# Performance work log

Measured on AMD Instinct MI355X. Metric: run time of the kernel, lower is better.

## Reference

```python
import jax, jax.numpy as jnp
import numpy as np
from jax import lax

V = 9; C1 = 80; C2 = 40; C4 = 24; CH = 32
H1, W1 = 30, 40; H2, W2 = 60, 80; H4, W4 = 120, 160
SHAPE = (96, 96, 96); N = 131072; EPS = 1e-5
OFFS = np.stack(np.meshgrid(np.arange(-1, 2), np.arange(-1, 2), np.arange(-1, 2), indexing='ij'), -1).reshape(-1, 3).astype(np.int32)  # 27 kernel offsets


def conv2d(x, w, b):
    y = lax.conv_general_dilated(x, w, (1, 1), 'SAME', dimension_numbers=('NCHW', 'OIHW', 'NCHW'))
    return y + b[None, :, None, None]


def bn1d(x, g, b):  # eval-mode BatchNorm1d (running_mean=0, running_var=1)
    return g * x * (1.0 / np.sqrt(1.0 + EPS)) + b


def layernorm(x, g, b):
    m = x.mean(-1, keepdims=True)
    v = ((x - m) ** 2).mean(-1, keepdims=True)
    return (x - m) / jnp.sqrt(v + EPS) * g + b


def grid_sample_zeros(img, gx, gy):
    # img [V,C,H,W]; gx,gy [V,M] normalized to [-1,1]; bilinear, align_corners=True, zeros padding
    Vn, C, H, W = img.shape
    px = (gx + 1.0) * 0.5 * (W - 1)
    py = (gy + 1.0) * 0.5 * (H - 1)
    x0 = jnp.floor(px); y0 = jnp.floor(py)
    wx = px - x0; wy = py - y0
    flat = img.reshape(Vn, C, H * W)
    def corner(xc, yc, wgt):
        valid = (xc >= 0) & (xc <= W - 1) & (yc >= 0) & (yc <= H - 1)
        xi = jnp.clip(xc, 0, W - 1).astype(jnp.int32)
        yi = jnp.clip(yc, 0, H - 1).astype(jnp.int32)
        idx = yi * W + xi  # [V,M]
        g = jax.vmap(lambda f, i: f[:, i])(flat, idx)  # [V,C,M]
        return g * (wgt * valid)[:, None, :]
    return (corner(x0, y0, (1 - wx) * (1 - wy)) + corner(x0 + 1, y0, wx * (1 - wy))
            + corner(x0, y0 + 1, (1 - wx) * wy) + corner(x0 + 1, y0 + 1, wx * wy))


def subm_conv(feat, W3, cxyz, grid):
    # submanifold sparse 3x3x3 conv: per-offset gather of active neighbors -> GEMM -> accumulate
    n = feat.shape[0]
    shp = jnp.asarray(SHAPE, jnp.int32)
    out = jnp.zeros((n, W3.shape[-1]), feat.dtype)
    for k in range(27):
        nc = cxyz + jnp.asarray(OFFS[k])
        inb = jnp.all((nc >= 0) & (nc < shp), axis=1)
        ncc = jnp.clip(nc, 0, shp - 1)
        idx = grid[ncc[:, 0], ncc[:, 1], ncc[:, 2]]
        ok = (inb & (idx >= 0)).astype(feat.dtype)
        g = feat[jnp.clip(idx, 0, n - 1)] * ok[:, None]
        out = out + g @ W3[k]
    return out


def _forward(feats_1x, feats_2x, feats_4x, origin, voxel_size, KRcam,
             w_f1, b_f1, w_f2, b_f2, w_f4, b_f4, w_down, b_down,
             w_p1, b_p1, w_p2, b_p2, w_p3, b_p3, w_p4, b_p4,
             bn0_g, bn0_b, w_elan, w_s1, ln1_g, ln1_b, w_s2, ln2_g, ln2_b,
             w_s3, ln3_g, ln3_b, w_s4, bn4_g, bn4_b,
             coords, stage, min_view_number):
    # feat_fusion_pre (bs=1, take batch 0)
    f1 = jax.nn.relu(conv2d(feats_1x[:, 0], w_f1, b_f1))
    f2 = jax.nn.relu(conv2d(feats_2x[:, 0], w_f2, b_f2))
    f4 = jax.nn.relu(conv2d(feats_4x[:, 0], w_f4, b_f4))
    f1 = jax.image.resize(f1, (V, C1, H2, W2), 'bilinear')  # F.interpolate x2
    f4 = f4.reshape(V, C4, H2, 2, W2, 2).mean(axis=(3, 5))  # AvgPool2d(2)
    fuse = jnp.concatenate([f1, f2, f4], axis=1)
    fuse = jax.nn.relu(conv2d(fuse, w_down, b_down))
    for w, b in ((w_p1, b_p1), (w_p2, b_p2), (w_p3, b_p3), (w_p4, b_p4)):
        fuse = fuse + jax.nn.relu(conv2d(fuse, w, b))  # residual blocks -> [V,CH,H2,W2]
    # multi-view projection
    cxyz = coords[:, 1:]
    world = cxyz.astype(jnp.float32) * voxel_size + origin[0]
    hom = jnp.concatenate([world, jnp.ones_like(world[:, :1])], axis=1)  # [N,4]
    im_p = jnp.einsum('vij,nj->vin', KRcam[:, 0], hom)  # [V,3,N]
    im_z = im_p[:, 2]
    gx = 2.0 * (im_p[:, 0] / im_z) / (W4 - 1) - 1.0
    gy = 2.0 * (im_p[:, 1] / im_z) / (H4 - 1) - 1.0
    mask = (jnp.abs(gx) <= 1) & (jnp.abs(gy) <= 1) & (im_z > 0)  # [V,N]
    count = mask.sum(0).astype(jnp.float32)
    # inputs are constructed so every voxel is seen by all views: valid_voxel compaction == identity
    feats = grid_sample_zeros(fuse, gx, gy) * mask[:, None, :]  # [V,CH,N]
    feat = feats.transpose(2, 0, 1)  # [N,V,CH]
    m = mask.T.astype(feat.dtype)  # [N,V]
    den = m.sum(1, keepdims=True)
    mean = (m[..., None] * feat).sum(1) / den
    var = (m[..., None] * (feat - mean[:, None, :]) ** 2).sum(1) / den  # [N,CH]
    # sparse subm conv chain
    sc = cxyz // (2 ** (2 - stage))  # stage=2 -> identity
    grid = jnp.full(SHAPE, -1, jnp.int32).at[sc[:, 0], sc[:, 1], sc[:, 2]].set(jnp.arange(N, dtype=jnp.int32))
    x = bn1d(var, bn0_g, bn0_b)
    x = jax.nn.relu(subm_conv(x, w_elan, sc, grid))  # Spares3dELAN stand-in
    r = jax.nn.relu(subm_conv(x, w_s1, sc, grid)); x = layernorm(r + x, ln1_g, ln1_b)
    r = jax.nn.relu(subm_conv(x, w_s2, sc, grid)); x = layernorm(r + x, ln2_g, ln2_b)
    r = jax.nn.relu(subm_conv(x, w_s3, sc, grid)); x = layernorm(r + x, ln3_g, ln3_b)
    occ = bn1d(subm_conv(x, w_s4, sc, grid), bn4_g, bn4_b)  # [N,1]
    return occ, coords, count


def setup_inputs() -> dict:
    key = jax.random.key(0)
    keys = jax.random.split(key, 40)
    ki = iter(range(40))
    def rn(shape, s=1.0):
        return jax.random.normal(keys[next(ki)], shape, jnp.float32) * s
    inp = {}
    inp['feats_1x'] = rn((V, 1, C1, H1, W1))
    inp['feats_2x'] = rn((V, 1, C2, H2, W2))
    inp['feats_4x'] = rn((V, 1, C4, H4, W4))
    flat = np.arange(N, dtype=np.int64) * 6  # unique active voxels in a 96^3 grid
    cx = flat // (96 * 96); rem = flat % (96 * 96)
    inp['coords'] = jnp.asarray(np.stack([np.zeros(N, np.int64), cx, rem // 96, rem % 96], 1), jnp.int32)
    inp['origin'] = jnp.asarray([[-1.92, -1.92, 1.0]], jnp.float32)
    inp['voxel_size'] = jnp.float32(0.04)
    fx, fy = 38.0, 28.0
    P = np.zeros((V, 1, 3, 4), np.float32)
    for v in range(V):
        P[v, 0] = np.array([[fx, 0.0, (W4 - 1) / 2, fx * 0.02 * (v - 4)],
                            [0.0, fy, (H4 - 1) / 2, 0.0],
                            [0.0, 0.0, 1.0, 0.0]], np.float32)
    inp['KRcam'] = jnp.asarray(P)
    s = 0.05
    inp['w_f1'] = rn((C1, C1, 3, 3), s); inp['b_f1'] = rn((C1,), s)
    inp['w_f2'] = rn((C2, C2, 3, 3), s); inp['b_f2'] = rn((C2,), s)
    inp['w_f4'] = rn((C4, C4, 3, 3), s); inp['b_f4'] = rn((C4,), s)
    inp['w_down'] = rn((CH, C1 + C2 + C4, 1, 1), s); inp['b_down'] = rn((CH,), s)
    for i in (1, 2, 3, 4):
        inp['w_p%d' % i] = rn((CH, CH, 3, 3), s); inp['b_p%d' % i] = rn((CH,), s)
    inp['bn0_g'] = jnp.ones((CH,), jnp.float32); inp['bn0_b'] = jnp.zeros((CH,), jnp.float32)
    inp['w_elan'] = rn((27, CH, CH), s)
    inp['w_s1'] = rn((27, CH, CH), s); inp['ln1_g'] = jnp.ones((CH,), jnp.float32); inp['ln1_b'] = jnp.zeros((CH,), jnp.float32)
    inp['w_s2'] = rn((27, CH, CH), s); inp['ln2_g'] = jnp.ones((CH,), jnp.float32); inp['ln2_b'] = jnp.zeros((CH,), jnp.float32)
    inp['w_s3'] = rn((27, CH, CH), s); inp['ln3_g'] = jnp.ones((CH,), jnp.float32); inp['ln3_b'] = jnp.zeros((CH,), jnp.float32)
    inp['w_s4'] = rn((27, CH, 1), s); inp['bn4_g'] = jnp.ones((1,), jnp.float32); inp['bn4_b'] = jnp.zeros((1,), jnp.float32)
    inp['stage'] = 2
    inp['min_view_number'] = 1
    return inp


def reference(feats_1x, feats_2x, feats_4x, origin, voxel_size, KRcam,
              w_f1, b_f1, w_f2, b_f2, w_f4, b_f4, w_down, b_down,
              w_p1, b_p1, w_p2, b_p2, w_p3, b_p3, w_p4, b_p4,
              bn0_g, bn0_b, w_elan, w_s1, ln1_g, ln1_b, w_s2, ln2_g, ln2_b,
              w_s3, ln3_g, ln3_b, w_s4, bn4_g, bn4_b,
              coords, stage, min_view_number):
    return _forward(feats_1x, feats_2x, feats_4x, origin, voxel_size, KRcam,
                    w_f1, b_f1, w_f2, b_f2, w_f4, b_f4, w_down, b_down,
                    w_p1, b_p1, w_p2, b_p2, w_p3, b_p3, w_p4, b_p4,
                    bn0_g, bn0_b, w_elan, w_s1, ln1_g, ln1_b, w_s2, ln2_g, ln2_b,
                    w_s3, ln3_g, ln3_b, w_s4, bn4_g, bn4_b,
                    coords, stage, min_view_number)
```

## Files before the change

### kernel.cpp

```cpp
#include <hip/hip_runtime.h>
#include <math.h>

#define VN 9
#define NVOX 131072
#define GS 96
static constexpr float INVS = 0.9999950000374997f;

typedef short bf16x8 __attribute__((ext_vector_type(8)));
typedef float f32x4v __attribute__((ext_vector_type(4)));

__device__ inline float4 ld4(const float* p){ return *reinterpret_cast<const float4*>(p); }

__device__ inline ushort f2b(float f){
  unsigned u = __float_as_uint(f);
  unsigned r = (u + 0x7fffu + ((u >> 16) & 1u)) >> 16;
  return (ushort)r;
}
__device__ inline float b2f(ushort s){ return __uint_as_float(((unsigned)s) << 16); }
__device__ inline float blo(unsigned u){ return __uint_as_float(u << 16); }
__device__ inline float bhi(unsigned u){ return __uint_as_float(u & 0xffff0000u); }

__device__ inline float4 ld4b(const ushort* p){
  uint2 u = *reinterpret_cast<const uint2*>(p);
  float4 r; r.x = blo(u.x); r.y = bhi(u.x); r.z = blo(u.y); r.w = bhi(u.y); return r;
// ... 60 lines not shown
}

__global__ __launch_bounds__(256) void k_prep(
    const float* wf1s, const float* wf2s, const float* wf4s, const float* wdns,
    const float* wp0s, const float* wp1s, const float* wp2s, const float* wp3s,
    const float* wes, const float* ws1s, const float* ws2s, const float* ws3s,
    ushort* wf1, ushort* wf2, ushort* wf4, ushort* wdn,
    ushort* wp0, ushort* wp1, ushort* wp2, ushort* wp3,
    ushort* w2e, ushort* w2s1, ushort* w2s2, ushort* w2s3,
    int* grid,
    const float* f1, const float* f2, const float* f4,
    ushort* o1, ushort* o2, ushort* o4){
  __shared__ float lds[96*65];
  int bid = blockIdx.x;
  int tx = threadIdx.x;
  if (bid < 270){ int t = bid*256+tx; if (t < 69120) wprep2_dev(wf1s, wf1, 80, 80, 3, 3, 80, t); return; }
  bid -= 270;
  if (bid < 108){ int t = bid*256+tx; if (t < 27648) wprep2_dev(wf2s, wf2, 40, 40, 3, 2, 48, t); return; }
  bid -= 108;
  if (bid < 36){ int t = bid*256+tx; if (t < 9216) wprep2_dev(wf4s, wf4, 24, 24, 3, 1, 32, t); return; }
  bid -= 36;
  if (bid < 20){ int t = bid*256+tx; if (t < 5120) wprep2_dev(wdns, wdn, 32, 144, 1, 5, 32, t); return; }
  bid -= 20;
  if (bid < 36){ int t = bid*256+tx; if (t < 9216) wprep2_dev(wp0s, wp0, 32, 32, 3, 1, 32, t); return; }
  bid -= 36;
  if (bid < 36){ int t = bid*256+tx; if (t < 9216) wprep2_dev(wp1s, wp1, 32, 32, 3, 1, 32, t); return; }
  bid -= 36;
  if (bid < 36){ int t = bid*256+tx; if (t < 9216) wprep2_dev(wp2s, wp2, 32, 32, 3, 1, 32, t); return; }
  bid -= 36;
  if (bid < 36){ int t = bid*256+tx; if (t < 9216) wprep2_dev(wp3s, wp3, 32, 32, 3, 1, 32, t); return; }
  bid -= 36;
  if (bid < 108){ int t = bid*256+tx; if (t < 27648) wprep_dev(wes, w2e, t); return; }
  bid -= 108;
  if (bid < 108){ int t = bid*256+tx; if (t < 27648) wprep_dev(ws1s, w2s1, t); return; }
  bid -= 108;
  if (bid < 108){ int t = bid*256+tx; if (t < 27648) wprep_dev(ws2s, w2s2, t); return; }
  bid -= 108;
  if (bid < 108){ int t = bid*256+tx; if (t < 27648) wprep_dev(ws3s, w2s3, t); return; }
  bid -= 108;
  if (bid < 3456){ int t = bid*256+tx; if (t < GS*GS*GS) grid[t] = -1; return; }
  bid -= 3456;
  if (bid < 171){ nhwc_tile_dev(f1, o1, 80, 96, 1200, bid, 19, lds, tx); return; }
  bid -= 171;
  if (bid < 675){ nhwc_tile_dev(f2, o2, 40, 64, 4800, bid, 75, lds, tx); return; }
  bid -= 675;
  if (bid < 2700){ nhwc_tile_dev(f4, o4, 24, 32, 19200, bid, 300, lds, tx); }
}

template<int CK, int NT, int TAPS, int MT>
__device__ void conv_dev(
    const ushort* __restrict__ fin, const ushort* __restrict__ w2,
    const float* __restrict__ bias, ushort* __restrict__ outp,
    int H, int W, int total, int Cout, int outStride, int outOff,
    const ushort* __restrict__ skipin, int bid, int tid){
  constexpr int CIN = CK*32;
  constexpr int COP = NT*16;
  int lane = tid & 63;
  int wave = tid >> 6;
  int vbase = bid*(MT*64) + wave*(MT*16);
  int m = lane & 15, q = lane >> 4;
  int HW = H*W;
  int p[MT], py[MT], px[MT]; bool pin[MT];
  #pragma unroll
  for (int t = 0; t < MT; ++t){
    int pp = vbase + t*16 + m;
    pin[t] = pp < total;
    if (pp > total-1) pp = total-1;
    p[t] = pp;
    int v = pp / HW; int rem = pp - v*HW;
    int y = rem / W;
    py[t] = y; px[t] = rem - y*W;
  }
  f32x4v acc[MT][NT];
  #pragma unroll
  for (int t = 0; t < MT; ++t)
    #pragma unroll
    for (int n = 0; n < NT; ++n) acc[t][n] = 0.f;
  bf16x8 z = (short)0;

  #pragma unroll 1
  for (int tap = 0; tap < TAPS; ++tap){
    int dy = (TAPS == 9) ? tap/3 - 1 : 0;
    int dx = (TAPS == 9) ? tap%3 - 1 : 0;
    int off = dy*W + dx;
    bool val[MT];
    #pragma unroll
    for (int t = 0; t < MT; ++t)
      val[t] = pin[t] && ((unsigned)(py[t]+dy) < (unsigned)H)
                      && ((unsigned)(px[t]+dx) < (unsigned)W);
    #pragma unroll
    for (int ck = 0; ck < CK; ++ck){
      bf16x8 Af[MT], Bf[NT];
      #pragma unroll
      for (int t = 0; t < MT; ++t){
        size_t idx = val[t] ? (size_t)(p[t]+off) : 0;
        bf16x8 a = *(const bf16x8*)(fin + idx*CIN + ck*32 + q*8);
        Af[t] = val[t] ? a : z;
      }
      #pragma unroll
      for (int n = 0; n < NT; ++n)
        Bf[n] = *(const bf16x8*)(w2 + ((size_t)((tap*CK+ck)*COP + n*16 + m))*32 + q*8);
      #pragma unroll
      for (int t = 0; t < MT; ++t)
        #pragma unroll
        for (int n = 0; n < NT; ++n)
          acc[t][n] = __builtin_amdgcn_mfma_f32_16x16x32_bf16(Af[t], Bf[n], acc[t][n], 0, 0, 0);
    }
  }

  #pragma unroll
  for (int n = 0; n < NT; ++n){
    int co = n*16 + m;
    bool cok = co < Cout;
    float bs = cok ? bias[co] : 0.f;
    #pragma unroll
    for (int t = 0; t < MT; ++t){
      #pragma unroll
      for (int r = 0; r < 4; ++r){
        int pp = vbase + t*16 + q*4 + r;
        if (pp < total && cok){
          float x = fmaxf(acc[t][n][r] + bs, 0.f);
          if (skipin) x += b2f(skipin[(size_t)pp*CIN + co]);
          outp[(size_t)pp*outStride + outOff + co] = f2b(x);
        }
      }
    }
  }
}

template<int CK, int NT, int TAPS, int MT>
__global__ __launch_bounds__(256) void k_conv_mfma(
    const ushort* __restrict__ fin, const ushort* __restrict__ w2,
    const float* __restrict__ bias, ushort* __restrict__ outp,
    int H, int W, int total, int Cout, int outStride, int outOff,
    const ushort* __restrict__ skipin){
  conv_dev<CK,NT,TAPS,MT>(fin, w2, bias, outp, H, W, total, Cout, outStride, outOff,
                          skipin, blockIdx.x, threadIdx.x);
}

template<int TH, int NT>
__device__ void conv_lds_dev(
    const ushort* __restrict__ fin, const ushort* __restrict__ w2,
    const float* __restrict__ bias, ushort* __restrict__ outp,
    int H, int W, int Cout, int outStride,
    const ushort* __restrict__ skipin, ushort* lds, int bid, int tid){
  constexpr int RPW = TH/4;
  constexpr int PS = 36;
  int xtiles = W >> 4;
  int ytiles = (H + TH - 1) / TH;
  int v  = bid / (ytiles*xtiles);
  int rem = bid - v*(ytiles*xtiles);
  int ty = (rem / xtiles) * TH;
  int tx = (rem % xtiles) * 16;
  const ushort* ibase = fin + (size_t)v*H*W*32;
  for (int i = tid; i < (TH+2)*18*4; i += 256){
    int chunk = i & 3;
    int pxi = i >> 2;
    int ly = pxi / 18, lx = pxi - ly*18;
    int gy = ty + ly - 1, gx = tx + lx - 1;
    uint4 d = {0,0,0,0};
    if ((unsigned)gy < (unsigned)H && (unsigned)gx < (unsigned)W)
      d = *(const uint4*)(ibase + ((size_t)gy*W + gx)*32 + chunk*8);
    *(uint4*)(lds + (size_t)(ly*18 + lx)*PS + chunk*8) = d;
  }
  __syncthreads();
  int lane = tid & 63;
  int wave = tid >> 6;
  int m = lane & 15, q = lane >> 4;
  f32x4v acc[RPW][NT];
  #pragma unroll
  for (int t = 0; t < RPW; ++t)
    #pragma unroll
    for (int n = 0; n < NT; ++n) acc[t][n] = 0.f;

  #pragma unroll 1
  for (int tap = 0; tap < 9; ++tap){
    int dy = tap/3 - 1, dx = tap%3 - 1;
    bf16x8 Af[RPW], Bf[NT];
    #pragma unroll
    for (int t = 0; t < RPW; ++t){
      int ly = wave*RPW + t + 1 + dy;
      int lx = m + 1 + dx;
      Af[t] = *(const bf16x8*)(lds + (size_t)(ly*18 + lx)*PS + q*8);
    }
    #pragma unroll
    for (int n = 0; n < NT; ++n)
      Bf[n] = *(const bf16x8*)(w2 + ((size_t)(tap*(NT*16) + n*16 + m))*32 + q*8);
    #pragma unroll
    for (int t = 0; t < RPW; ++t)
      #pragma unroll
      for (int n = 0; n < NT; ++n)
        acc[t][n] = __builtin_amdgcn_mfma_f32_16x16x32_bf16(Af[t], Bf[n], acc[t][n], 0, 0, 0);
  }

  #pragma unroll
  for (int n = 0; n < NT; ++n){
    int co = n*16 + m;
    bool cok = co < Cout;
    float bs = cok ? bias[co] : 0.f;
    #pragma unroll
    for (int t = 0; t < RPW; ++t){
      int y = ty + wave*RPW + t;
      #pragma unroll
      for (int r = 0; r < 4; ++r){
        int x = tx + q*4 + r;
        if (y < H && cok){
          size_t pp = (size_t)(v*H + y)*W + x;
          float val = fmaxf(acc[t][n][r] + bs, 0.f);
          if (skipin) val += b2f(skipin[pp*32 + co]);
          outp[pp*outStride + co] = f2b(val);
        }
      }
    }
  }
}

__global__ __launch_bounds__(256) void k_conv_lds4(
    const ushort* __restrict__ fin, const ushort* __restrict__ w2,
    const float* __restrict__ bias, ushort* __restrict__ outp,
    const ushort* __restrict__ skipin){
  __shared__ ushort lds[6*18*36];
  conv_lds_dev<4,2>(fin, w2, bias, outp, 60, 80, 32, 32, skipin, lds, blockIdx.x, threadIdx.x);
}

__device__ void scatter_dev(const int* __restrict__ coords, const int* __restrict__ stage,
                            int* __restrict__ grid, int* __restrict__ scn,
                            float* __restrict__ coords_out,
                            const float* __restrict__ origin, const float* __restrict__ vsz,
                            const float* __restrict__ KR,
                            ushort* __restrict__ sidx, uint2* __restrict__ sw,
                            float* __restrict__ cnt, int n){
  int c0 = coords[n*4], c1 = coords[n*4+1], c2 = coords[n*4+2], c3 = coords[n*4+3];
  coords_out[n*4+0] = (float)c0;
  coords_out[n*4+1] = (float)c1;
  coords_out[n*4+2] = (float)c2;
  coords_out[n*4+3] = (float)c3;
  int sh = 2 - stage[0];
  int s1 = c1 >> sh, s2 = c2 >> sh, s3 = c3 >> sh;
  scn[n*3+0] = s1; scn[n*3+1] = s2; scn[n*3+2] = s3;
  grid[(s1*GS + s2)*GS + s3] = n;

  float vs = vsz[0];
  float wx = (float)c1*vs + origin[0];
  float wy = (float)c2*vs + origin[1];
  float wz = (float)c3*vs + origin[2];
  float den = 0.f;
  #pragma unroll 1
  for (int v = 0; v < VN; ++v){
    const float* P = KR + v*12;
    float ix = P[0]*wx + P[1]*wy + P[2]*wz + P[3];
    float iy = P[4]*wx + P[5]*wy + P[6]*wz + P[7];
    float iz = P[8]*wx + P[9]*wy + P[10]*wz + P[11];
    float gx = 2.f*(ix/iz)/159.f - 1.f;
    float gy = 2.f*(iy/iz)/119.f - 1.f;
    bool ok = (fabsf(gx) <= 1.f) && (fabsf(gy) <= 1.f) && (iz > 0.f);
    float px = ok ? (gx + 1.f)*0.5f*79.f : 0.f;
    float py = ok ? (gy + 1.f)*0.5f*59.f : 0.f;
    float x0f = floorf(px), y0f = floorf(py);
    float fx = px - x0f, fy = py - y0f;
    int idx = (int)y0f*80 + (int)x0f;
    float mf = ok ? 1.f : 0.f;
    float w00 = (1.f-fx)*(1.f-fy)*mf, w01 = fx*(1.f-fy)*mf;
    float w10 = (1.f-fx)*fy*mf,       w11 = fx*fy*mf;
    uint2 s;
    s.x = (unsigned)f2b(w00) | ((unsigned)f2b(w01) << 16);
    s.y = (unsigned)f2b(w10) | ((unsigned)f2b(w11) << 16);
    sidx[(size_t)v*NVOX + n] = (ushort)idx;
    sw[(size_t)v*NVOX + n] = s;
    den += mf;
  }
  cnt[n] = den;
}

__global__ __launch_bounds__(256) void k_heads(
    const ushort* nhwc1, const ushort* wf1, const float* b_f1, ushort* t1,
    const ushort* nhwc2, const ushort* wf2, const float* b_f2, ushort* fcat,
    const ushort* nhwc4, const ushort* wf4, const float* b_f4, ushort* t4,
    const int* coords, const int* stage, int* grid, int* scn, float* coords_out,
    const float* origin, const float* vsz, const float* KR,
    ushort* sidx, uint2* sw, float* cnt){
  __shared__ ushort lds[18*18*36];
  int bid = blockIdx.x;
  int tid = threadIdx.x;
  if (bid < 169){ conv_dev<3,5,9,1>(nhwc1, wf1, b_f1, t1, 30, 40, 10800, 80, 80, 0, nullptr, bid, tid); return; }
  bid -= 169;
  if (bid < 720){ conv_lds_dev<16,2>(nhwc4, wf4, b_f4, t4, 120, 160, 24, 24, nullptr, lds, bid, tid); return; }
  bid -= 720;
  if (bid < 675){ conv_dev<2,3,9,1>(nhwc2, wf2, b_f2, fcat, 60, 80, 43200, 40, 160, 80, nullptr, bid, tid); return; }
  bid -= 675;
  { int n = bid*256 + tid;
    scatter_dev(coords, stage, grid, scn, coords_out, origin, vsz, KR, sidx, sw, cnt, n); }
}

__global__ __launch_bounds__(256) void k_respool_nbr(
    const ushort* __restrict__ t1, const ushort* __restrict__ t4, ushort* __restrict__ fc,
    const int* __restrict__ scn, const int* __restrict__ grid,
    int* __restrict__ nbr, unsigned* __restrict__ gmask16){
  __shared__ unsigned m16[4];
  int bid = blockIdx.x;
  int tidx = threadIdx.x;
  if (bid < 5063){
    int tid = bid*256 + tidx;
    if (tid < 864000){
      int c4 = tid % 20;
      int x  = (tid / 20) % 80;
      int y  = (tid / 1600) % 60;
      int v  = tid / 96000;
      int c = c4*4;
      int ky = y >> 1; int y0, y1; float wy0, wy1;
      if ((y & 1) == 0){ y0 = ky-1; y1 = ky; wy0 = 0.25f; wy1 = 0.75f; if (y0 < 0){ y0 = 0; wy0 = 0.f; wy1 = 1.f; } }
      else             { y0 = ky; y1 = ky+1; wy0 = 0.75f; wy1 = 0.25f; if (y1 > 29){ y1 = 29; wy1 = 0.f; wy0 = 1.f; } }
      int kx = x >> 1; int x0, x1; float wx0, wx1;
      if ((x & 1) == 0){ x0 = kx-1; x1 = kx; wx0 = 0.25f; wx1 = 0.75f; if (x0 < 0){ x0 = 0; wx0 = 0.f; wx1 = 1.f; } }
      else             { x0 = kx; x1 = kx+1; wx0 = 0.75f; wx1 = 0.25f; if (x1 > 39){ x1 = 39; wx1 = 0.f; wx0 = 1.f; } }
      float4 a00 = ld4b(t1 + ((size_t)(v*30 + y0)*40 + x0)*80 + c);
      float4 a01 = ld4b(t1 + ((size_t)(v*30 + y0)*40 + x1)*80 + c);
      float4 a10 = ld4b(t1 + ((size_t)(v*30 + y1)*40 + x0)*80 + c);
      float4 a11 = ld4b(t1 + ((size_t)(v*30 + y1)*40 + x1)*80 + c);
      float w00 = wy0*wx0, w01 = wy0*wx1, w10 = wy1*wx0, w11 = wy1*wx1;
      float4 r;
      r.x = w00*a00.x + w01*a01.x + w10*a10.x + w11*a11.x;
      r.y = w00*a00.y + w01*a01.y + w10*a10.y + w11*a11.y;
      r.z = w00*a00.z + w01*a01.z + w10*a10.z + w11*a11.z;
      r.w = w00*a00.w + w01*a01.w + w10*a10.w + w11*a11.w;
      st4b(fc + ((size_t)(v*60 + y)*80 + x)*160 + c, r);
      return;
    }
    int t = tid - 864000;
    if (t >= 432000) return;
    int c4 = t % 10;
    int x  = (t / 10) % 80;
    int y  = (t / 800) % 60;
    int v  = t / 48000;
    if (c4 < 6){
      int c = c4*4;
      const ushort* b0 = t4 + ((size_t)(v*120 + 2*y)*160 + 2*x)*24 + c;
      float4 a = ld4b(b0), b = ld4b(b0 + 24), cc = ld4b(b0 + 160*24), d = ld4b(b0 + 160*24 + 24);
      float4 r;
      r.x = 0.25f*(a.x + b.x + cc.x + d.x);
      r.y = 0.25f*(a.y + b.y + cc.y + d.y);
      r.z = 0.25f*(a.z + b.z + cc.z + d.z);
      r.w = 0.25f*(a.w + b.w + cc.w + d.w);
      st4b(fc + ((size_t)(v*60 + y)*80 + x)*160 + 120 + c, r);
    } else {
      float4 zz = {0.f,0.f,0.f,0.f};
      st4b(fc + ((size_t)(v*60 + y)*80 + x)*160 + 144 + (c4-6)*4, zz);
    }
    return;
  }
  bid -= 5063;
  if (tidx < 4) m16[tidx] = 0;
  __syncthreads();
  int vb = bid*64;
  int lane = tidx & 63;
  int wv = tidx >> 6;
  int n = vb + lane;
  int sx = scn[n*3+0], sy = scn[n*3+1], sz = scn[n*3+2];
  int k0 = wv*7;
  int k1 = min(27, k0 + 7);
  unsigned msk = 0;
  #pragma unroll 1
  for (int k = k0; k < k1; ++k){
    int dx = k/9 - 1, dy = (k/3)%3 - 1, dz = k%3 - 1;
    int nx = sx+dx, ny = sy+dy, nz = sz+dz;
    int idx = -1;
    if (((unsigned)nx < 96u) && ((unsigned)ny < 96u) && ((unsigned)nz < 96u))
      idx = grid[(nx*GS + ny)*GS + nz];
    unsigned long long b = __ballot(idx >= 0);
    unsigned sub = (unsigned)((b >> ((lane >> 4)*16)) & 0xFFFFull);
    if (sub){
      nbr[(size_t)k*NVOX + n] = idx;
      msk |= (1u << k);
    }
  }
  if ((lane & 15) == 0 && msk) atomicOr(&m16[lane >> 4], msk);
  __syncthreads();
  if (tidx < 4) gmask16[(vb >> 4) + tidx] = m16[tidx];
}

__global__ __launch_bounds__(256) void k_sample(
    const ushort* __restrict__ fuse, const ushort* __restrict__ sidx,
    const uint2* __restrict__ sw,
    const float* __restrict__ cnt, const float* __restrict__ bn0g,
    const float* __restrict__ bn0b, ushort* __restrict__ F0){
  int tid = blockIdx.x*256 + threadIdx.x;
  int vox = tid >> 3;
  int c4 = tid & 7;
  int c = c4*4;
  int si[VN]; uint2 wv[VN];
  #pragma unroll
  for (int v = 0; v < VN; ++v){
    si[v] = sidx[(size_t)v*NVOX + vox];
    wv[v] = sw[(size_t)v*NVOX + vox];
  }
  float s0=0.f,s1=0.f,s2=0.f,s3=0.f;
  float q0=0.f,q1=0.f,q2=0.f,q3=0.f;
  #pragma unroll
  for (int v = 0; v < VN; ++v){
    float w00 = blo(wv[v].x), w01 = bhi(wv[v].x);
    float w10 = blo(wv[v].y), w11 = bhi(wv[v].y);
    const ushort* bp = fuse + (size_t)v*153600 + (size_t)si[v]*32 + c;
    float4 a00 = ld4b(bp);
    float4 a01 = ld4b(bp + 32);
    float4 a10 = ld4b(bp + 2560);
    float4 a11 = ld4b(bp + 2592);
    float g0 = w00*a00.x + w01*a01.x + w10*a10.x + w11*a11.x;
    float g1 = w00*a00.y + w01*a01.y + w10*a10.y + w11*a11.y;
    float g2 = w00*a00.z + w01*a01.z + w10*a10.z + w11*a11.z;
    float g3 = w00*a00.w + w01*a01.w + w10*a10.w + w11*a11.w;
    s0 += g0; q0 += g0*g0;
    s1 += g1; q1 += g1*g1;
    s2 += g2; q2 += g2*g2;
    s3 += g3; q3 += g3*g3;
  }
  float iden = 1.f/cnt[vox];
  float m0 = s0*iden, m1 = s1*iden, m2 = s2*iden, m3 = s3*iden;
  float4 g = ld4(bn0g + c);
  float4 b = ld4(bn0b + c);
  float4 r;
  r.x = g.x*fmaxf(q0*iden - m0*m0, 0.f)*INVS + b.x;
  r.y = g.y*fmaxf(q1*iden - m1*m1, 0.f)*INVS + b.y;
  r.z = g.z*fmaxf(q2*iden - m2*m2, 0.f)*INVS + b.z;
  r.w = g.w*fmaxf(q3*iden - m3*m3, 0.f)*INVS + b.w;
  st4b(F0 + (size_t)vox*32 + c, r);
}

template<int MODE>
__global__ __launch_bounds__(256, 4) void k_subm_mfma(
    const ushort* __restrict__ fin, const ushort* __restrict__ w2,
    const int* __restrict__ nbr, const unsigned* __restrict__ gmask16,
    const float* __restrict__ lng, const float* __restrict__ lnb,
    ushort* __restrict__ fout){
  int lane = threadIdx.x & 63;
  int wave = threadIdx.x >> 6;
  int vb = blockIdx.x*128 + wave*32;
  int m = lane & 15;
  int q = lane >> 4;

  unsigned rem0 = gmask16[(vb >> 4) + 0];
  unsigned rem1 = gmask16[(vb >> 4) + 1];
  unsigned rem = rem0 | rem1;

  f32x4v acc[2][2];
  acc[0][0] = 0.f; acc[0][1] = 0.f; acc[1][0] = 0.f; acc[1][1] = 0.f;
  bf16x8 zc = (short)0;

  while (rem){
    int k0 = __ffs(rem) - 1; rem &= rem - 1;
    int k1 = -1, k2 = -1;
    if (rem){ k1 = __ffs(rem) - 1; rem &= rem - 1; }
    if (rem){ k2 = __ffs(rem) - 1; rem &= rem - 1; }
    int a0v = nbr[(size_t)k0*NVOX + vb + m];
    int b0v = nbr[(size_t)k0*NVOX + vb + 16 + m];
    int a1 = -1, b1 = -1, a2 = -1, b2 = -1;
    if (k1 >= 0){
      int av = nbr[(size_t)k1*NVOX + vb + m];
      int bv = nbr[(size_t)k1*NVOX + vb + 16 + m];
      a1 = ((rem0 >> k1) & 1) ? av : -1;
      b1 = ((rem1 >> k1) & 1) ? bv : -1;
    }
    if (k2 >= 0){
      int av = nbr[(size_t)k2*NVOX + vb + m];
      int bv = nbr[(size_t)k2*NVOX + vb + 16 + m];
      a2 = ((rem0 >> k2) & 1) ? av : -1;
      b2 = ((rem1 >> k2) & 1) ? bv : -1;
    }
    int a0 = ((rem0 >> k0) & 1) ? a0v : -1;
    int b0 = ((rem1 >> k0) & 1) ? b0v : -1;
    bf16x8 A0, B0, A1 = zc, B1 = zc, A2 = zc, B2 = zc, t;
    bf16x8 w10 = zc, w11 = zc, w20 = zc, w21 = zc;
    t = *(const bf16x8*)(fin + (size_t)(a0 < 0 ? 0 : a0)*32 + q*8); A0 = (a0 < 0) ? zc : t;
    t = *(const bf16x8*)(fin + (size_t)(b0 < 0 ? 0 : b0)*32 + q*8); B0 = (b0 < 0) ? zc : t;
    bf16x8 w00 = *(const bf16x8*)(w2 + (size_t)(k0*32 + m)*32 + q*8);
    bf16x8 w01 = *(const bf16x8*)(w2 + (size_t)(k0*32 + 16 + m)*32 + q*8);
    if (k1 >= 0){
      t = *(const bf16x8*)(fin + (size_t)(a1 < 0 ? 0 : a1)*32 + q*8); A1 = (a1 < 0) ? zc : t;
      t = *(const bf16x8*)(fin + (size_t)(b1 < 0 ? 0 : b1)*32 + q*8); B1 = (b1 < 0) ? zc : t;
      w10 = *(const bf16x8*)(w2 + (size_t)(k1*32 + m)*32 + q*8);
      w11 = *(const bf16x8*)(w2 + (size_t)(k1*32 + 16 + m)*32 + q*8);
    }
    if (k2 >= 0){
      t = *(const bf16x8*)(fin + (size_t)(a2 < 0 ? 0 : a2)*32 + q*8); A2 = (a2 < 0) ? zc : t;
      t = *(const bf16x8*)(fin + (size_t)(b2 < 0 ? 0 : b2)*32 + q*8); B2 = (b2 < 0) ? zc : t;
      w20 = *(const bf16x8*)(w2 + (size_t)(k2*32 + m)*32 + q*8);
      w21 = *(const bf16x8*)(w2 + (size_t)(k2*32 + 16 + m)*32 + q*8);
    }
    acc[0][0] = __builtin_amdgcn_mfma_f32_16x16x32_bf16(A0, w00, acc[0][0], 0, 0, 0);
    acc[0][1] = __builtin_amdgcn_mfma_f32_16x16x32_bf16(A0, w01, acc[0][1], 0, 0, 0);
    acc[1][0] = __builtin_amdgcn_mfma_f32_16x16x32_bf16(B0, w00, acc[1][0], 0, 0, 0);
    acc[1][1] = __builtin_amdgcn_mfma_f32_16x16x32_bf16(B0, w01, acc[1][1], 0, 0, 0);
    if (k1 >= 0){
      acc[0][0] = __builtin_amdgcn_mfma_f32_16x16x32_bf16(A1, w10, acc[0][0], 0, 0, 0);
      acc[0][1] = __builtin_amdgcn_mfma_f32_16x16x32_bf16(A1, w11, acc[0][1], 0, 0, 0);
      acc[1][0] = __builtin_amdgcn_mfma_f32_16x16x32_bf16(B1, w10, acc[1][0], 0, 0, 0);
      acc[1][1] = __builtin_amdgcn_mfma_f32_16x16x32_bf16(B1, w11, acc[1][1], 0, 0, 0);
    }
    if (k2 >= 0){
      acc[0][0] = __builtin_amdgcn_mfma_f32_16x16x32_bf16(A2, w20, acc[0][0], 0, 0, 0);
      acc[0][1] = __builtin_amdgcn_mfma_f32_16x16x32_bf16(A2, w21, acc[0][1], 0, 0, 0);
      acc[1][0] = __builtin_amdgcn_mfma_f32_16x16x32_bf16(B2, w20, acc[1][0], 0, 0, 0);
      acc[1][1] = __builtin_amdgcn_mfma_f32_16x16x32_bf16(B2, w21, acc[1][1], 0, 0, 0);
    }
  }

  int ch0 = m, ch1 = 16 + m;
  float g0 = 0.f, g1 = 0.f, bb0 = 0.f, bb1 = 0.f;
  if (MODE == 1){ g0 = lng[ch0]; g1 = lng[ch1]; bb0 = lnb[ch0]; bb1 = lnb[ch1]; }
  #pragma unroll
  for (int t = 0; t < 2; ++t){
    #pragma unroll
    for (int r = 0; r < 4; ++r){
      int vox = vb + t*16 + q*4 + r;
      float x0 = fmaxf(acc[t][0][r], 0.f);
      float x1 = fmaxf(acc[t][1][r], 0.f);
      if (MODE == 1){
        x0 += b2f(fin[(size_t)vox*32 + ch0]);
        x1 += b2f(fin[(size_t)vox*32 + ch1]);
        float s = x0 + x1;
        s += __shfl_xor(s, 1, 16);
        s += __shfl_xor(s, 2, 16);
        s += __shfl_xor(s, 4, 16);
        s += __shfl_xor(s, 8, 16);
        float mean = s * (1.f/32.f);
        float d0 = x0 - mean, d1 = x1 - mean;
        float v2 = d0*d0 + d1*d1;
        v2 += __shfl_xor(v2, 1, 16);
        v2 += __shfl_xor(v2, 2, 16);
        v2 += __shfl_xor(v2, 4, 16);
        v2 += __shfl_xor(v2, 8, 16);
        float rs = 1.f / sqrtf(v2*(1.f/32.f) + 1e-5f);
        x0 = d0*rs*g0 + bb0;
        x1 = d1*rs*g1 + bb1;
      }
      fout[(size_t)vox*32 + ch0] = f2b(x0);
      fout[(size_t)vox*32 + ch1] = f2b(x1);
    }
  }
}

__global__ __launch_bounds__(256) void k_s4(
    const ushort* __restrict__ fin, const float* __restrict__ w4,
    const int* __restrict__ nbr, const unsigned* __restrict__ gmask16,
    const float* __restrict__ bn4g, const float* __restrict__ bn4b,
    float* __restrict__ occ){
  int tid = blockIdx.x*256 + threadIdx.x;
  int n = tid >> 2;
  int part = tid & 3;
  unsigned rem = gmask16[n >> 4];
  float acc = 0.f;
  while (rem){
    int k0 = __ffs(rem) - 1; rem &= rem - 1;
    int k1 = -1;
    if (rem){ k1 = __ffs(rem) - 1; rem &= rem - 1; }
    int i0 = nbr[(size_t)k0*NVOX + n];
    int i1 = (k1 >= 0) ? nbr[(size_t)k1*NVOX + n] : -1;
    uint4 d0 = *(const uint4*)(fin + (size_t)(i0 < 0 ? 0 : i0)*32 + part*8);
    uint4 d1 = {0,0,0,0};
    if (k1 >= 0) d1 = *(const uint4*)(fin + (size_t)(i1 < 0 ? 0 : i1)*32 + part*8);
    if (i0 >= 0){
      float4 wa = ld4(w4 + k0*32 + part*8);
      float4 wb = ld4(w4 + k0*32 + part*8 + 4);
      acc += blo(d0.x)*wa.x + bhi(d0.x)*wa.y + blo(d0.y)*wa.z + bhi(d0.y)*wa.w
           + blo(d0.z)*wb.x + bhi(d0.z)*wb.y + blo(d0.w)*wb.z + bhi(d0.w)*wb.w;
    }
    if (i1 >= 0){
      float4 wa = ld4(w4 + k1*32 + part*8);
      float4 wb = ld4(w4 + k1*32 + part*8 + 4);
      acc += blo(d1.x)*wa.x + bhi(d1.x)*wa.y + blo(d1.y)*wa.z + bhi(d1.y)*wa.w
           + blo(d1.z)*wb.x + bhi(d1.z)*wb.y + blo(d1.w)*wb.z + bhi(d1.w)*wb.w;
    }
  }
  acc += __shfl_xor(acc, 1, 4);
  acc += __shfl_xor(acc, 2, 4);
  if (part == 0) occ[n] = bn4g[0]*acc*INVS + bn4b[0];
}

extern "C" void kernel_launch(void* const* d_in, const int* in_sizes, int n_in,
                              void* d_out, int out_size, void* d_ws, size_t ws_size,
                              hipStream_t stream){
  const float* feats1 = (const float*)d_in[0];
  const float* feats2 = (const float*)d_in[1];
  const float* feats4 = (const float*)d_in[2];
  const int*   coords = (const int*)d_in[3];
  const float* origin = (const float*)d_in[4];
  const float* vsz    = (const float*)d_in[5];
  const float* KR     = (const float*)d_in[6];
  const float* w_f1 = (const float*)d_in[7];  const float* b_f1 = (const float*)d_in[8];
  const float* w_f2 = (const float*)d_in[9];  const float* b_f2 = (const float*)d_in[10];
  const float* w_f4 = (const float*)d_in[11]; const float* b_f4 = (const float*)d_in[12];
  const float* w_dn = (const float*)d_in[13]; const float* b_dn = (const float*)d_in[14];
  const float* w_p[4] = {(const float*)d_in[15], (const float*)d_in[17],
                         (const float*)d_in[19], (const float*)d_in[21]};
  const float* b_p[4] = {(const float*)d_in[16], (const float*)d_in[18],
                         (const float*)d_in[20], (const float*)d_in[22]};
  const float* bn0g = (const float*)d_in[23]; const float* bn0b = (const float*)d_in[24];
  const float* w_elan = (const float*)d_in[25];
  const float* w_s1 = (const float*)d_in[26]; const float* ln1g = (const float*)d_in[27]; const float* ln1b = (const float*)d_in[28];
  const float* w_s2 = (const float*)d_in[29]; const float* ln2g = (const float*)d_in[30]; const float* ln2b = (const float*)d_in[31];
  const float* w_s3 = (const float*)d_in[32]; const float* ln3g = (const float*)d_in[33]; const float* ln3b = (const float*)d_in[34];
  const float* w_s4 = (const float*)d_in[35]; const float* bn4g = (const float*)d_in[36]; const float* bn4b = (const float*)d_in[37];
  const int* stage  = (const int*)d_in[38];
  float* out = (float*)d_out;
  char* base = (char*)d_ws;

  size_t off = 0;
  auto alloc = [&](size_t bytes)->char*{ char* p = base + off; off += (bytes + 255) & ~(size_t)255; return p; };
  ushort* nhwc1 = (ushort*)alloc((size_t)9*30*40*96*2);
  ushort* nhwc2 = (ushort*)alloc((size_t)9*60*80*64*2);
  ushort* nhwc4 = (ushort*)alloc((size_t)9*120*160*32*2);
  ushort* t1    = (ushort*)alloc((size_t)9*30*40*80*2);
  ushort* t4    = (ushort*)alloc((size_t)9*120*160*24*2);
  ushort* fcat  = (ushort*)alloc((size_t)9*60*80*160*2);
  ushort* A     = (ushort*)alloc((size_t)9*60*80*32*2);
  ushort* B     = (ushort*)alloc((size_t)9*60*80*32*2);
  ushort* Fb0   = (ushort*)alloc((size_t)NVOX*32*2);
  ushort* Fb1   = (ushort*)alloc((size_t)NVOX*32*2);
  int*    nbr   = (int*)alloc((size_t)27*NVOX*4);
  int*    grid  = (int*)alloc((size_t)GS*GS*GS*4);
  int*    scn   = (int*)alloc((size_t)NVOX*3*4);
  unsigned* gmask16 = (unsigned*)alloc((size_t)(NVOX/16)*4);
  ushort* wf1   = (ushort*)alloc(9*3*80*32*2);
  ushort* wf2   = (ushort*)alloc(9*2*48*32*2);
  ushort* wf4   = (ushort*)alloc(9*1*32*32*2);
  ushort* wdn   = (ushort*)alloc(1*5*32*32*2);
  ushort* wp0   = (ushort*)alloc(9*1*32*32*2);
  ushort* wp1   = (ushort*)alloc(9*1*32*32*2);
  ushort* wp2   = (ushort*)alloc(9*1*32*32*2);
  ushort* wp3   = (ushort*)alloc(9*1*32*32*2);
  ushort* w2e   = (ushort*)alloc(27*1024*2);
  ushort* w2s1  = (ushort*)alloc(27*1024*2);
  ushort* w2s2  = (ushort*)alloc(27*1024*2);
  ushort* w2s3  = (ushort*)alloc(27*1024*2);
  ushort* sidx  = (ushort*)alloc((size_t)VN*NVOX*2);
  uint2*  sw    = (uint2*)alloc((size_t)VN*NVOX*8);

  auto nb = [](int total){ return (total + 255)/256; };

  k_prep<<<8012,256,0,stream>>>(
      w_f1, w_f2, w_f4, w_dn, w_p[0], w_p[1], w_p[2], w_p[3],
      w_elan, w_s1, w_s2, w_s3,
      wf1, wf2, wf4, wdn, wp0, wp1, wp2, wp3, w2e, w2s1, w2s2, w2s3, grid,
      feats1, feats2, feats4, nhwc1, nhwc2, nhwc4);

  k_heads<<<169 + 720 + 675 + 512,256,0,stream>>>(
      nhwc1, wf1, b_f1, t1,
      nhwc2, wf2, b_f2, fcat,
      nhwc4, wf4, b_f4, t4,
      coords, stage, grid, scn, out + NVOX,
      origin, vsz, KR, sidx, sw, out + 5*NVOX);

  k_respool_nbr<<<5063 + 2048,256,0,stream>>>(t1, t4, fcat, scn, grid, nbr, gmask16);

  k_conv_mfma<5,2,1,1><<<675,256,0,stream>>>(fcat, wdn, b_dn, A, 60, 80, 43200, 32, 32, 0, nullptr);
  k_conv_lds4<<<675,256,0,stream>>>(A, wp0, b_p[0], B, A);
  k_conv_lds4<<<675,256,0,stream>>>(B, wp1, b_p[1], A, B);
  k_conv_lds4<<<675,256,0,stream>>>(A, wp2, b_p[2], B, A);
  k_conv_lds4<<<675,256,0,stream>>>(B, wp3, b_p[3], A, B);

  k_sample<<<NVOX/32,256,0,stream>>>(A, sidx, sw, out + 5*NVOX, bn0g, bn0b, Fb0);

  k_subm_mfma<0><<<NVOX/128,256,0,stream>>>(Fb0, w2e,  nbr, gmask16, nullptr, nullptr, Fb1);
  k_subm_mfma<1><<<NVOX/128,256,0,stream>>>(Fb1, w2s1, nbr, gmask16, ln1g, ln1b, Fb0);
  k_subm_mfma<1><<<NVOX/128,256,0,stream>>>(Fb0, w2s2, nbr, gmask16, ln2g, ln2b, Fb1);
  k_subm_mfma<1><<<NVOX/128,256,0,stream>>>(Fb1, w2s3, nbr, gmask16, ln3g, ln3b, Fb0);

  k_s4<<<NVOX/64,256,0,stream>>>(Fb0, w_s4, nbr, gmask16, bn4g, bn4b, out);
}
```

Measured before the change: 343.9 us.

## Transpose MFMA operands for vectorized epilogues; recompute sample weights inline

The MFMA operand order is swapped in the dense conv, LDS conv and sparse subm kernels. Each lane now holds four consecutive output channels for one pixel or voxel, so the epilogues do 8-byte bf16 vector stores, vector bias/LN-parameter loads and vector skip loads instead of scalar strided ones. The LayerNorm reduction now uses two cross-quad shuffles instead of four. Separately, the scatter stage no longer precomputes and stores the bilinear sample indices and weights; k_sample recomputes the projection per voxel. This removes a global write/read round trip of sidx/sw at the cost of redundant projection math across the 8 threads sharing a voxel.

New measurement: 345.2 us. No clear change (+0.4%).

```diff
diff --git a/kernel.cpp b/kernel.cpp
--- a/kernel.cpp
+++ b/kernel.cpp
@@ -136,7 +136,7 @@
     const ushort* __restrict__ fin, const ushort* __restrict__ w2,
     const float* __restrict__ bias, ushort* __restrict__ outp,
     int H, int W, int total, int Cout, int outStride, int outOff,
-    const ushort* __restrict__ skipin, int bid, int tid){
+    int bid, int tid){
   constexpr int CIN = CK*32;
   constexpr int COP = NT*16;
   int lane = tid & 63;
@@ -188,25 +188,25 @@
       for (int t = 0; t < MT; ++t)
         #pragma unroll
         for (int n = 0; n < NT; ++n)
-          acc[t][n] = __builtin_amdgcn_mfma_f32_16x16x32_bf16(Af[t], Bf[n], acc[t][n], 0, 0, 0);
+          acc[t][n] = __builtin_amdgcn_mfma_f32_16x16x32_bf16(Bf[n], Af[t], acc[t][n], 0, 0, 0);
     }
   }
 
   #pragma unroll
   for (int n = 0; n < NT; ++n){
-    int co = n*16 + m;
-    bool cok = co < Cout;
-    float bs = cok ? bias[co] : 0.f;
+    int co4 = n*16 + q*4;
+    bool cok = co4 < Cout;
+    float4 bs = cok ? ld4(bias + co4) : float4{0.f,0.f,0.f,0.f};
     #pragma unroll
     for (int t = 0; t < MT; ++t){
-      #pragma unroll
-      for (int r = 0; r < 4; ++r){
-        int pp = vbase + t*16 + q*4 + r;
-        if (pp < total && cok){
-          float x = fmaxf(acc[t][n][r] + bs, 0.f);
-          if (skipin) x += b2f(skipin[(size_t)pp*CIN + co]);
-          outp[(size_t)pp*outStride + outOff + co] = f2b(x);
-        }
+      int pp = vbase + t*16 + m;
+      if (pp < total && cok){
+        float4 v;
+        v.x = fmaxf(acc[t][n][0] + bs.x, 0.f);
+        v.y = fmaxf(acc[t][n][1] + bs.y, 0.f);
+        v.z = fmaxf(acc[t][n][2] + bs.z, 0.f);
+        v.w = fmaxf(acc[t][n][3] + bs.w, 0.f);
+        st4b(outp + (size_t)pp*outStride + outOff + co4, v);
       }
     }
   }
@@ -216,10 +216,9 @@
 __global__ __launch_bounds__(256) void k_conv_mfma(
     const ushort* __restrict__ fin, const ushort* __restrict__ w2,
     const float* __restrict__ bias, ushort* __restrict__ outp,
-    int H, int W, int total, int Cout, int outStride, int outOff,
-    const ushort* __restrict__ skipin){
+    int H, int W, int total, int Cout, int outStride, int outOff){
   conv_dev<CK,NT,TAPS,MT>(fin, w2, bias, outp, H, W, total, Cout, outStride, outOff,
-                          skipin, blockIdx.x, threadIdx.x);
+                          blockIdx.x, threadIdx.x);
 }
 
 template<int TH, int NT>
@@ -274,26 +273,30 @@
     for (int t = 0; t < RPW; ++t)
       #pragma unroll
       for (int n = 0; n < NT; ++n)
-        acc[t][n] = __builtin_amdgcn_mfma_f32_16x16x32_bf16(Af[t], Bf[n], acc[t][n], 0, 0, 0);
+        acc[t][n] = __builtin_amdgcn_mfma_f32_16x16x32_bf16(Bf[n], Af[t], acc[t][n], 0, 0, 0);
   }
 
   #pragma unroll
   for (int n = 0; n < NT; ++n){
-    int co = n*16 + m;
-    bool cok = co < Cout;
-    float bs = cok ? bias[co] : 0.f;
+    int co4 = n*16 + q*4;
+    bool cok = co4 < Cout;
+    float4 bs = cok ? ld4(bias + co4) : float4{0.f,0.f,0.f,0.f};
     #pragma unroll
     for (int t = 0; t < RPW; ++t){
       int y = ty + wave*RPW + t;
-      #pragma unroll
-      for (int r = 0; r < 4; ++r){
-        int x = tx + q*4 + r;
-        if (y < H && cok){
-          size_t pp = (size_t)(v*H + y)*W + x;
-          float val = fmaxf(acc[t][n][r] + bs, 0.f);
-          if (skipin) val += b2f(skipin[pp*32 + co]);
-          outp[pp*outStride + co] = f2b(val);
+      int x = tx + m;
+      if (y < H && cok){
+        size_t pp = (size_t)(v*H + y)*W + x;
+        float4 val;
+        val.x = fmaxf(acc[t][n][0] + bs.x, 0.f);
+        val.y = fmaxf(acc[t][n][1] + bs.y, 0.f);
+        val.z = fmaxf(acc[t][n][2] + bs.z, 0.f);
+        val.w = fmaxf(acc[t][n][3] + bs.w, 0.f);
+        if (skipin){
+          float4 sk = ld4b(skipin + pp*32 + co4);
+          val.x += sk.x; val.y += sk.y; val.z += sk.z; val.w += sk.w;
         }
+        st4b(outp + pp*outStride + co4, val);
       }
     }
   }
@@ -312,7 +315,6 @@
                             float* __restrict__ coords_out,
                             const float* __restrict__ origin, const float* __restrict__ vsz,
                             const float* __restrict__ KR,
-                            ushort* __restrict__ sidx, uint2* __restrict__ sw,
                             float* __restrict__ cnt, int n){
   int c0 = coords[n*4], c1 = coords[n*4+1], c2 = coords[n*4+2], c3 = coords[n*4+3];
   coords_out[n*4+0] = (float)c0;
@@ -338,20 +340,7 @@
     float gx = 2.f*(ix/iz)/159.f - 1.f;
     float gy = 2.f*(iy/iz)/119.f - 1.f;
     bool ok = (fabsf(gx) <= 1.f) && (fabsf(gy) <= 1.f) && (iz > 0.f);
-    float px = ok ? (gx + 1.f)*0.5f*79.f : 0.f;
-    float py = ok ? (gy + 1.f)*0.5f*59.f : 0.f;
-    float x0f = floorf(px), y0f = floorf(py);
-    float fx = px - x0f, fy = py - y0f;
-    int idx = (int)y0f*80 + (int)x0f;
-    float mf = ok ? 1.f : 0.f;
-    float w00 = (1.f-fx)*(1.f-fy)*mf, w01 = fx*(1.f-fy)*mf;
-    float w10 = (1.f-fx)*fy*mf,       w11 = fx*fy*mf;
-    uint2 s;
-    s.x = (unsigned)f2b(w00) | ((unsigned)f2b(w01) << 16);
-    s.y = (unsigned)f2b(w10) | ((unsigned)f2b(w11) << 16);
-    sidx[(size_t)v*NVOX + n] = (ushort)idx;
-    sw[(size_t)v*NVOX + n] = s;
-    den += mf;
+    den += ok ? 1.f : 0.f;
   }
   cnt[n] = den;
 }
@@ -361,19 +350,18 @@
     const ushort* nhwc2, const ushort* wf2, const float* b_f2, ushort* fcat,
     const ushort* nhwc4, const ushort* wf4, const float* b_f4, ushort* t4,
     const int* coords, const int* stage, int* grid, int* scn, float* coords_out,
-    const float* origin, const float* vsz, const float* KR,
-    ushort* sidx, uint2* sw, float* cnt){
+    const float* origin, const float* vsz, const float* KR, float* cnt){
   __shared__ ushort lds[18*18*36];
   int bid = blockIdx.x;
   int tid = threadIdx.x;
-  if (bid < 169){ conv_dev<3,5,9,1>(nhwc1, wf1, b_f1, t1, 30, 40, 10800, 80, 80, 0, nullptr, bid, tid); return; }
+  if (bid < 169){ conv_dev<3,5,9,1>(nhwc1, wf1, b_f1, t1, 30, 40, 10800, 80, 80, 0, bid, tid); return; }
   bid -= 169;
   if (bid < 720){ conv_lds_dev<16,2>(nhwc4, wf4, b_f4, t4, 120, 160, 24, 24, nullptr, lds, bid, tid); return; }
   bid -= 720;
-  if (bid < 675){ conv_dev<2,3,9,1>(nhwc2, wf2, b_f2, fcat, 60, 80, 43200, 40, 160, 80, nullptr, bid, tid); return; }
+  if (bid < 675){ conv_dev<2,3,9,1>(nhwc2, wf2, b_f2, fcat, 60, 80, 43200, 40, 160, 80, bid, tid); return; }
   bid -= 675;
   { int n = bid*256 + tid;
-    scatter_dev(coords, stage, grid, scn, coords_out, origin, vsz, KR, sidx, sw, cnt, n); }
+    scatter_dev(coords, stage, grid, scn, coords_out, origin, vsz, KR, cnt, n); }
 }
 
 __global__ __launch_bounds__(256) void k_respool_nbr(
@@ -463,27 +451,42 @@
 }
 
 __global__ __launch_bounds__(256) void k_sample(
-    const ushort* __restrict__ fuse, const ushort* __restrict__ sidx,
-    const uint2* __restrict__ sw,
-    const float* __restrict__ cnt, const float* __restrict__ bn0g,
+    const ushort* __restrict__ fuse, const int* __restrict__ coords,
+    const float* __restrict__ origin, const float* __restrict__ vsz,
+    const float* __restrict__ KR,
+    const float* __restrict__ bn0g,
     const float* __restrict__ bn0b, ushort* __restrict__ F0){
   int tid = blockIdx.x*256 + threadIdx.x;
   int vox = tid >> 3;
   int c4 = tid & 7;
   int c = c4*4;
-  int si[VN]; uint2 wv[VN];
+  int c1 = coords[vox*4+1], c2 = coords[vox*4+2], c3 = coords[vox*4+3];
+  float vs = vsz[0];
+  float wxx = (float)c1*vs + origin[0];
+  float wyy = (float)c2*vs + origin[1];
+  float wzz = (float)c3*vs + origin[2];
+  float s0=0.f,s1=0.f,s2=0.f,s3=0.f;
+  float q0=0.f,q1=0.f,q2=0.f,q3=0.f;
+  float den = 0.f;
   #pragma unroll
   for (int v = 0; v < VN; ++v){
-    si[v] = sidx[(size_t)v*NVOX + vox];
-    wv[v] = sw[(size_t)v*NVOX + vox];
-  }
-  float s0=0.f,s1=0.f,s2=0.f,s3=0.f;
-  float q0=0.f,q1=0.f,q2=0.f,q3=0.f;
-  #pragma unroll
-  for (int v = 0; v < VN; ++v){
-    float w00 = blo(wv[v].x), w01 = bhi(wv[v].x);
-    float w10 = blo(wv[v].y), w11 = bhi(wv[v].y);
-    const ushort* bp = fuse + (size_t)v*153600 + (size_t)si[v]*32 + c;
+    const float* P = KR + v*12;
+    float ix = P[0]*wxx + P[1]*wyy + P[2]*wzz + P[3];
+    float iy = P[4]*wxx + P[5]*wyy + P[6]*wzz + P[7];
+    float iz = P[8]*wxx + P[9]*wyy + P[10]*wzz + P[11];
+    float gx = 2.f*(ix/iz)/159.f - 1.f;
+    float gy = 2.f*(iy/iz)/119.f - 1.f;
+    bool ok = (fabsf(gx) <= 1.f) && (fabsf(gy) <= 1.f) && (iz > 0.f);
+    float px = ok ? (gx + 1.f)*0.5f*79.f : 0.f;
+    float py = ok ? (gy + 1.f)*0.5f*59.f : 0.f;
+    float x0f = floorf(px), y0f = floorf(py);
+    float fx = px - x0f, fy = py - y0f;
+    int idx = (int)y0f*80 + (int)x0f;
+    float mf = ok ? 1.f : 0.f;
+    den += mf;
+    float w00 = (1.f-fx)*(1.f-fy)*mf, w01 = fx*(1.f-fy)*mf;
+    float w10 = (1.f-fx)*fy*mf,       w11 = fx*fy*mf;
+    const ushort* bp = fuse + (size_t)v*153600 + (size_t)idx*32 + c;
     float4 a00 = ld4b(bp);
     float4 a01 = ld4b(bp + 32);
     float4 a10 = ld4b(bp + 2560);
@@ -497,7 +500,7 @@
     s2 += g2; q2 += g2*g2;
     s3 += g3; q3 += g3*g3;
   }
-  float iden = 1.f/cnt[vox];
+  float iden = 1.f/den;
   float m0 = s0*iden, m1 = s1*iden, m2 = s2*iden, m3 = s3*iden;
   float4 g = ld4(bn0g + c);
   float4 b = ld4(bn0b + c);
@@ -569,56 +572,63 @@
       w20 = *(const bf16x8*)(w2 + (size_t)(k2*32 + m)*32 + q*8);
       w21 = *(const bf16x8*)(w2 + (size_t)(k2*32 + 16 + m)*32 + q*8);
     }
-    acc[0][0] = __builtin_amdgcn_mfma_f32_16x16x32_bf16(A0, w00, acc[0][0], 0, 0, 0);
-    acc[0][1] = __builtin_amdgcn_mfma_f32_16x16x32_bf16(A0, w01, acc[0][1], 0, 0, 0);
-    acc[1][0] = __builtin_amdgcn_mfma_f32_16x16x32_bf16(B0, w00, acc[1][0], 0, 0, 0);
-    acc[1][1] = __builtin_amdgcn_mfma_f32_16x16x32_bf16(B0, w01, acc[1][1], 0, 0, 0);
+    acc[0][0] = __builtin_amdgcn_mfma_f32_16x16x32_bf16(w00, A0, acc[0][0], 0, 0, 0);
+    acc[0][1] = __builtin_amdgcn_mfma_f32_16x16x32_bf16(w01, A0, acc[0][1], 0, 0, 0);
+    acc[1][0] = __builtin_amdgcn_mfma_f32_16x16x32_bf16(w00, B0, acc[1][0], 0, 0, 0);
+    acc[1][1] = __builtin_amdgcn_mfma_f32_16x16x32_bf16(w01, B0, acc[1][1], 0, 0, 0);
     if (k1 >= 0){
-      acc[0][0] = __builtin_amdgcn_mfma_f32_16x16x32_bf16(A1, w10, acc[0][0], 0, 0, 0);
-      acc[0][1] = __builtin_amdgcn_mfma_f32_16x16x32_bf16(A1, w11, acc[0][1], 0, 0, 0);
-      acc[1][0] = __builtin_amdgcn_mfma_f32_16x16x32_bf16(B1, w10, acc[1][0], 0, 0, 0);
-      acc[1][1] = __builtin_amdgcn_mfma_f32_16x16x32_bf16(B1, w11, acc[1][1], 0, 0, 0);
+      acc[0][0] = __builtin_amdgcn_mfma_f32_16x16x32_bf16(w10, A1, acc[0][0], 0, 0, 0);
+      acc[0][1] = __builtin_amdgcn_mfma_f32_16x16x32_bf16(w11, A1, acc[0][1], 0, 0, 0);
+      acc[1][0] = __builtin_amdgcn_mfma_f32_16x16x32_bf16(w10, B1, acc[1][0], 0, 0, 0);
+      acc[1][1] = __builtin_amdgcn_mfma_f32_16x16x32_bf16(w11, B1, acc[1][1], 0, 0, 0);
     }
     if (k2 >= 0){
-      acc[0][0] = __builtin_amdgcn_mfma_f32_16x16x32_bf16(A2, w20, acc[0][0], 0, 0, 0);
-      acc[0][1] = __builtin_amdgcn_mfma_f32_16x16x32_bf16(A2, w21, acc[0][1], 0, 0, 0);
-      acc[1][0] = __builtin_amdgcn_mfma_f32_16x16x32_bf16(B2, w20, acc[1][0], 0, 0, 0);
-      acc[1][1] = __builtin_amdgcn_mfma_f32_16x16x32_bf16(B2, w21, acc[1][1], 0, 0, 0);
-    }
-  }
-
-  int ch0 = m, ch1 = 16 + m;
-  float g0 = 0.f, g1 = 0.f, bb0 = 0.f, bb1 = 0.f;
-  if (MODE == 1){ g0 = lng[ch0]; g1 = lng[ch1]; bb0 = lnb[ch0]; bb1 = lnb[ch1]; }
+      acc[0][0] = __builtin_amdgcn_mfma_f32_16x16x32_bf16(w20, A2, acc[0][0], 0, 0, 0);
+      acc[0][1] = __builtin_amdgcn_mfma_f32_16x16x32_bf16(w21, A2, acc[0][1], 0, 0, 0);
+      acc[1][0] = __builtin_amdgcn_mfma_f32_16x16x32_bf16(w20, B2, acc[1][0], 0, 0, 0);
+      acc[1][1] = __builtin_amdgcn_mfma_f32_16x16x32_bf16(w21, B2, acc[1][1], 0, 0, 0);
+    }
+  }
+
+  float4 g0v{0,0,0,0}, g1v{0,0,0,0}, b0v{0,0,0,0}, b1v{0,0,0,0};
+  if (MODE == 1){
+    g0v = ld4(lng + q*4);  g1v = ld4(lng + 16 + q*4);
+    b0v = ld4(lnb + q*4);  b1v = ld4(lnb + 16 + q*4);
+  }
   #pragma unroll
   for (int t = 0; t < 2; ++t){
+    int vox = vb + t*16 + m;
+    float x0[4], x1[4];
     #pragma unroll
     for (int r = 0; r < 4; ++r){
-      int vox = vb + t*16 + q*4 + r;
-      float x0 = fmaxf(acc[t][0][r], 0.f);
-      float x1 = fmaxf(acc[t][1][r], 0.f);
-      if (MODE == 1){
-        x0 += b2f(fin[(size_t)vox*32 + ch0]);
-        x1 += b2f(fin[(size_t)vox*32 + ch1]);
-        float s = x0 + x1;
-        s += __shfl_xor(s, 1, 16);
-        s += __shfl_xor(s, 2, 16);
-        s += __shfl_xor(s, 4, 16);
-        s += __shfl_xor(s, 8, 16);
-        float mean = s * (1.f/32.f);
-        float d0 = x0 - mean, d1 = x1 - mean;
-        float v2 = d0*d0 + d1*d1;
-        v2 += __shfl_xor(v2, 1, 16);
-        v2 += __shfl_xor(v2, 2, 16);
-        v2 += __shfl_xor(v2, 4, 16);
-        v2 += __shfl_xor(v2, 8, 16);
-        float rs = 1.f / sqrtf(v2*(1.f/32.f) + 1e-5f);
-        x0 = d0*rs*g0 + bb0;
-        x1 = d1*rs*g1 + bb1;
+      x0[r] = fmaxf(acc[t][0][r], 0.f);
+      x1[r] = fmaxf(acc[t][1][r], 0.f);
+    }
+    if (MODE == 1){
+      uint2 sk0 = *(const uint2*)(fin + (size_t)vox*32 + q*4);
+      uint2 sk1 = *(const uint2*)(fin + (size_t)vox*32 + 16 + q*4);
+      x0[0] += blo(sk0.x); x0[1] += bhi(sk0.x); x0[2] += blo(sk0.y); x0[3] += bhi(sk0.y);
+      x1[0] += blo(sk1.x); x1[1] += bhi(sk1.x); x1[2] += blo(sk1.y); x1[3] += bhi(sk1.y);
+      float s = (x0[0]+x0[1]+x0[2]+x0[3]) + (x1[0]+x1[1]+x1[2]+x1[3]);
+      s += __shfl_xor(s, 16);
+      s += __shfl_xor(s, 32);
+      float mean = s * (1.f/32.f);
+      float v2 = 0.f;
+      #pragma unroll
+      for (int r = 0; r < 4; ++r){
+        x0[r] -= mean; x1[r] -= mean;
+        v2 += x0[r]*x0[r] + x1[r]*x1[r];
       }
-      fout[(size_t)vox*32 + ch0] = f2b(x0);
-      fout[(size_t)vox*32 + ch1] = f2b(x1);
-    }
+      v2 += __shfl_xor(v2, 16);
+      v2 += __shfl_xor(v2, 32);
+      float rs = 1.f / sqrtf(v2*(1.f/32.f) + 1e-5f);
+      x0[0] = x0[0]*rs*g0v.x + b0v.x; x0[1] = x0[1]*rs*g0v.y + b0v.y;
+      x0[2] = x0[2]*rs*g0v.z + b0v.z; x0[3] = x0[3]*rs*g0v.w + b0v.w;
+      x1[0] = x1[0]*rs*g1v.x + b1v.x; x1[1] = x1[1]*rs*g1v.y + b1v.y;
+      x1[2] = x1[2]*rs*g1v.z + b1v.z; x1[3] = x1[3]*rs*g1v.w + b1v.w;
+    }
+    st4b(fout + (size_t)vox*32 + q*4,      float4{x0[0],x0[1],x0[2],x0[3]});
+    st4b(fout + (size_t)vox*32 + 16 + q*4, float4{x1[0],x1[1],x1[2],x1[3]});
   }
 }
 
@@ -715,8 +725,6 @@
   ushort* w2s1  = (ushort*)alloc(27*1024*2);
   ushort* w2s2  = (ushort*)alloc(27*1024*2);
   ushort* w2s3  = (ushort*)alloc(27*1024*2);
-  ushort* sidx  = (ushort*)alloc((size_t)VN*NVOX*2);
-  uint2*  sw    = (uint2*)alloc((size_t)VN*NVOX*8);
 
   auto nb = [](int total){ return (total + 255)/256; };
 
@@ -731,17 +739,17 @@
       nhwc2, wf2, b_f2, fcat,
       nhwc4, wf4, b_f4, t4,
       coords, stage, grid, scn, out + NVOX,
-      origin, vsz, KR, sidx, sw, out + 5*NVOX);
+      origin, vsz, KR, out + 5*NVOX);
 
   k_respool_nbr<<<5063 + 2048,256,0,stream>>>(t1, t4, fcat, scn, grid, nbr, gmask16);
 
-  k_conv_mfma<5,2,1,1><<<675,256,0,stream>>>(fcat, wdn, b_dn, A, 60, 80, 43200, 32, 32, 0, nullptr);
+  k_conv_mfma<5,2,1,1><<<675,256,0,stream>>>(fcat, wdn, b_dn, A, 60, 80, 43200, 32, 32, 0);
   k_conv_lds4<<<675,256,0,stream>>>(A, wp0, b_p[0], B, A);
   k_conv_lds4<<<675,256,0,stream>>>(B, wp1, b_p[1], A, B);
   k_conv_lds4<<<675,256,0,stream>>>(A, wp2, b_p[2], B, A);
   k_conv_lds4<<<675,256,0,stream>>>(B, wp3, b_p[3], A, B);
 
-  k_sample<<<NVOX/32,256,0,stream>>>(A, sidx, sw, out + 5*NVOX, bn0g, bn0b, Fb0);
+  k_sample<<<NVOX/32,256,0,stream>>>(A, coords, origin, vsz, KR, bn0g, bn0b, Fb0);
 
   k_subm_mfma<0><<<NVOX/128,256,0,stream>>>(Fb0, w2e,  nbr, gmask16, nullptr, nullptr, Fb1);
   k_subm_mfma<1><<<NVOX/128,256,0,stream>>>(Fb1, w2s1, nbr, gmask16, ln1g, ln1b, Fb0);
```
